# Optimization experiments

Hardware: AMD Instinct MI355X
Metric: run time of the kernel (lower is better)

## Reference

```python
import jax, jax.numpy as jnp
import numpy as np

H = 30  # hidden size
D_IN = 4
D_OUT = 4


def setup_inputs() -> dict:
    key = jax.random.key(0)
    ks = jax.random.split(key, 12)
    s = 0.1
    inp = {
        "input": jax.random.normal(ks[0], (2048, 1024, D_IN), dtype=jnp.float32),
        "W_ih1": jax.random.normal(ks[1], (4 * H, D_IN), dtype=jnp.float32) * s,
        "b_ih1": jax.random.normal(ks[2], (4 * H,), dtype=jnp.float32) * s,
        "W_hh1": jax.random.normal(ks[3], (4 * H, H), dtype=jnp.float32) * s,
        "b_hh1": jax.random.normal(ks[4], (4 * H,), dtype=jnp.float32) * s,
        "W_ih2": jax.random.normal(ks[5], (4 * H, H), dtype=jnp.float32) * s,
        "b_ih2": jax.random.normal(ks[6], (4 * H,), dtype=jnp.float32) * s,
        "W_hh2": jax.random.normal(ks[7], (4 * H, H), dtype=jnp.float32) * s,
        "b_hh2": jax.random.normal(ks[8], (4 * H,), dtype=jnp.float32) * s,
        "W_lin": jax.random.normal(ks[9], (D_OUT, H), dtype=jnp.float32) * s,
        "b_lin": jax.random.normal(ks[10], (D_OUT,), dtype=jnp.float32) * s,
        "future": 0,
    }
    return inp


def _lstm_cell(x, h, c, W_ih, b_ih, W_hh, b_hh):
    # PyTorch LSTMCell gate order: i, f, g, o
    gates = x @ W_ih.T + b_ih + h @ W_hh.T + b_hh  # [B, 4H]
    i, f, g, o = jnp.split(gates, 4, axis=-1)
    i = jax.nn.sigmoid(i)
    f = jax.nn.sigmoid(f)
    g = jnp.tanh(g)
    o = jax.nn.sigmoid(o)
    c_new = f * c + i * g
    h_new = o * jnp.tanh(c_new)
    return h_new, c_new


def reference(input, W_ih1, b_ih1, W_hh1, b_hh1, W_ih2, b_ih2, W_hh2, b_hh2,
              W_lin, b_lin, future):
    B, T, _ = input.shape

    def step(carry, x_t):
        h1, c1, h2, c2 = carry
        h1, c1 = _lstm_cell(x_t[:, :D_IN], h1, c1, W_ih1, b_ih1, W_hh1, b_hh1)
        h2, c2 = _lstm_cell(h1, h2, c2, W_ih2, b_ih2, W_hh2, b_hh2)
        out = h2 @ W_lin.T + b_lin  # [B, 4]
        return (h1, c1, h2, c2), out

    z = jnp.zeros((B, H), dtype=input.dtype)
    carry0 = (z, z, z, z)
    carry, outs = jax.lax.scan(step, carry0, jnp.transpose(input, (1, 0, 2)))
    outputs = jnp.transpose(outs, (1, 0, 2))  # [B, T, 4]

    if future > 0:
        h1, c1, h2, c2 = carry
        out = outputs[:, -1, :]
        fut = []
        for _ in range(future):
            h1, c1 = _lstm_cell(out, h1, c1, W_ih1, b_ih1, W_hh1, b_hh1)
            h2, c2 = _lstm_cell(h1, h2, c2, W_ih2, b_ih2, W_hh2, b_hh2)
            out = h2 @ W_lin.T + b_lin
            fut.append(out)
        outputs = jnp.concatenate([outputs, jnp.stack(fut, axis=1)], axis=1)
    return outputs
```

## Files before the change

kernel.cpp:

```cpp
#include <hip/hip_runtime.h>

typedef float f32x4 __attribute__((ext_vector_type(4)));
typedef float v4f  __attribute__((ext_vector_type(4)));
typedef _Float16 half8 __attribute__((ext_vector_type(8)));
typedef unsigned int u32;
typedef unsigned short u16;

#define HH 30
#define DIN 4
#define DOUT 4
#define NB 16
#define L2E 1.44269504088896340736f

#if __has_builtin(__builtin_amdgcn_exp2f)
#define EXP2F(v) __builtin_amdgcn_exp2f(v)
#else
#define EXP2F(v) exp2f(v)
#endif

__device__ __forceinline__ float sig2f(float v) {
    return __builtin_amdgcn_rcpf(1.0f + EXP2F(v));
}

__device__ __forceinline__ f32x4 MF(half8 a, half8 b, f32x4 c) {
    return __builtin_amdgcn_mfma_f32_16x16x32_f16(a, b, c, 0, 0, 0);
}

union F8 { half8 h; _Float16 e[8]; u32 w[4]; };
union HU { _Float16 h; u16 s; };

__device__ __forceinline__ void lds_barrier() {
    __builtin_amdgcn_sched_barrier(0);
    asm volatile("s_waitcnt lgkmcnt(0)" ::: "memory");
    __builtin_amdgcn_sched_barrier(0);
    __builtin_amdgcn_s_barrier();
    __builtin_amdgcn_sched_barrier(0);
}

__global__ __launch_bounds__(1024)
void lstm2_kernel(const float* __restrict__ x,
                  const float* __restrict__ Wih1, const float* __restrict__ bih1,
                  const float* __restrict__ Whh1, const float* __restrict__ bhh1,
                  const float* __restrict__ Wih2, const float* __restrict__ bih2,
                  const float* __restrict__ Whh2, const float* __restrict__ bhh2,
                  const float* __restrict__ Wlin, const float* __restrict__ blin,
                  float* __restrict__ out, int T)
{
    const int tid = threadIdx.x;
    const int w = tid >> 6;
    const int wt = w & 7;
    const bool isL2 = (w >= 8);
    const int l = tid & 63;
    const int n = l & 15;
    const int p = l >> 4;
    const int b0 = blockIdx.x * NB;
    const float M2 = -2.0f * L2E;

    __shared__ __align__(16) u16 lds[2][4][16][40];
    {
        u32* z = reinterpret_cast<u32*>(&lds[0][0][0][0]);
        const int tot = 2 * 4 * 16 * 40 / 2;
        for (int i = tid; i < tot; i += 1024) z[i] = 0u;
    }

    const int gA = n & 3;
    const float scA = (gA == 2) ? -2.0f * L2E : -L2E;
    const int qA = 4 * wt + (n >> 2);
    const int kq = 4 * wt + p;
    const bool okq = (kq < HH);
    const int kqc = okq ? kq : 0;
    const int pos = ((kq & 15) >> 2) * 8 + (kq >> 4) * 4 + (kq & 3);

    half8 wA_h0, wA_l0, wA_h1, wA_l1;
    {
        F8 H0, L0, H1, L1v;
#pragma unroll
        for (int e = 0; e < 8; ++e) {
            const int k = 16 * (e >> 2) + 4 * p + (e & 3);
            const bool kok = (qA < HH && k < HH);
            float v0, v1;
            if (isL2) {
                v0 = kok ? Wih2[(gA * HH + qA) * HH + k] * scA : 0.0f;
                v1 = kok ? Whh2[(gA * HH + qA) * HH + k] * scA : 0.0f;
            } else {
                v0 = kok ? Whh1[(gA * HH + qA) * HH + k] * scA : 0.0f;
                v1 = 0.0f;
            }
            _Float16 t0 = (_Float16)v0, t1 = (_Float16)v1;
            H0.e[e] = t0; L0.e[e] = (_Float16)(v0 - (float)t0);
            H1.e[e] = t1; L1v.e[e] = (_Float16)(v1 - (float)t1);
        }
        wA_h0 = H0.h; wA_l0 = L0.h; wA_h1 = H1.h; wA_l1 = L1v.h;
    }

    f32x4 biasf;
#pragma unroll
    for (int r = 0; r < 4; ++r) {
        const float scr = (r == 2) ? -2.0f * L2E : -L2E;
        const float bv = isL2 ? (bih2[r * HH + kqc] + bhh2[r * HH + kqc])
                              : (bih1[r * HH + kqc] + bhh1[r * HH + kqc]);
        biasf[r] = okq ? bv * scr : 0.0f;
    }

    float wxs[4][DIN];
#pragma unroll
    for (int r = 0; r < 4; ++r) {
        const float scr = (r == 2) ? -2.0f * L2E : -L2E;
#pragma unroll
        for (int c = 0; c < DIN; ++c)
            wxs[r][c] = (!isL2 && okq) ? Wih1[(r * HH + kqc) * DIN + c] * scr : 0.0f;
    }

    half8 alin_h, alin_l;
    f32x4 blinf;
    {
        F8 Lh, Ll;
#pragma unroll
        for (int e = 0; e < 8; ++e) {
            const int k = 16 * (e >> 2) + 4 * p + (e & 3);
            float v = (isL2 && n < DOUT && k < HH) ? Wlin[n * HH + k] : 0.0f;
            _Float16 t16 = (_Float16)v;
            Lh.e[e] = t16; Ll.e[e] = (_Float16)(v - (float)t16);
        }
        alin_h = Lh.h; alin_l = Ll.h;
#pragma unroll
        for (int r = 0; r < 4; ++r)
            blinf[r] = (p == 0) ? blin[r] : 0.0f;
    }

    float cst = 0.0f;
    half8 bh1_h = {}, bh1_l = {}, bh2_h = {}, bh2_l = {};

    const v4f* xp = reinterpret_cast<const v4f*>(x) + (size_t)(b0 + n) * T;

    f32x4 gx_cur = biasf;
    v4f xn = {};
    if (!isL2) {
        const v4f x0 = xp[0];
#pragma unroll
        for (int r = 0; r < 4; ++r)
#pragma unroll
            for (int c = 0; c < DIN; ++c)
                gx_cur[r] = fmaf(wxs[r][c], x0[c], gx_cur[r]);
        xn = xp[(T > 1) ? 1 : 0];
    }

    __syncthreads();

    const f32x4 zf = {0.0f, 0.0f, 0.0f, 0.0f};
    const int TS = T + 2;

    for (int s = 0; s < TS; ++s) {
        if (!isL2) {
            f32x4 a = MF(wA_h0, bh1_h, gx_cur);
            f32x4 b = MF(wA_h0, bh1_l, zf);
            f32x4 c = MF(wA_l0, bh1_h, zf);
            const f32x4 g = (a + b) + c;

            const float iv = sig2f(g[0]);
            const float fv = sig2f(g[1]);
            const float gg = fmaf(2.0f, sig2f(g[2]), -1.0f);
            const float ov = sig2f(g[3]);
            cst = fmaf(fv, cst, iv * gg);
            const float r = sig2f(M2 * cst);
            const float hn = fmaf(2.0f * ov, r, -ov);

            HU hi, lo;
            hi.h = (_Float16)hn;
            lo.h = (_Float16)(hn - (float)hi.h);
            lds[s & 1][0][n][pos] = okq ? hi.s : (u16)0;
            lds[s & 1][1][n][pos] = okq ? lo.s : (u16)0;
        } else {
            if (s >= 1) {
                f32x4 a = MF(wA_h0, bh1_h, biasf);
                f32x4 b = MF(wA_h0, bh1_l, zf);
                f32x4 c = MF(wA_l0, bh1_h, zf);
                f32x4 d = MF(wA_h1, bh2_h, zf);
                f32x4 e = MF(wA_h1, bh2_l, zf);
                f32x4 f = MF(wA_l1, bh2_h, zf);
                const f32x4 g = ((a + b) + (c + d)) + (e + f);

                const float iv = sig2f(g[0]);
                const float fv = sig2f(g[1]);
                const float gg = fmaf(2.0f, sig2f(g[2]), -1.0f);
                const float ov = sig2f(g[3]);
                cst = fmaf(fv, cst, iv * gg);
                const float r = sig2f(M2 * cst);
                const float hn = fmaf(2.0f * ov, r, -ov);

                HU hi, lo;
                hi.h = (_Float16)hn;
                lo.h = (_Float16)(hn - (float)hi.h);
                lds[(s + 1) & 1][2][n][pos] = okq ? hi.s : (u16)0;
                lds[(s + 1) & 1][3][n][pos] = okq ? lo.s : (u16)0;
            }
            if (s >= 2 && w == 8 + (s & 7)) {
                f32x4 oh = blinf;
                oh = MF(alin_h, bh2_h, oh);
                oh = MF(alin_h, bh2_l, oh);
                oh = MF(alin_l, bh2_h, oh);
                if (p == 0) {
                    v4f ov4;
                    ov4.x = oh[0]; ov4.y = oh[1]; ov4.z = oh[2]; ov4.w = oh[3];
                    *reinterpret_cast<v4f*>(
                        out + (((size_t)(b0 + n)) * T + (s - 2)) * DOUT) = ov4;
                }
            }
        }

        lds_barrier();

        bh1_h = *reinterpret_cast<const half8*>(&lds[s & 1][0][n][8 * p]);
        bh1_l = *reinterpret_cast<const half8*>(&lds[s & 1][1][n][8 * p]);
        if (isL2) {
            bh2_h = *reinterpret_cast<const half8*>(&lds[(s + 1) & 1][2][n][8 * p]);
            bh2_l = *reinterpret_cast<const half8*>(&lds[(s + 1) & 1][3][n][8 * p]);
        } else {
            f32x4 gxn = biasf;
#pragma unroll
            for (int r = 0; r < 4; ++r)
#pragma unroll
                for (int c = 0; c < DIN; ++c)
                    gxn[r] = fmaf(wxs[r][c], xn[c], gxn[r]);
            gx_cur = gxn;
            xn = xp[(s + 2 < T) ? (s + 2) : (T - 1)];
        }
    }
}

extern "C" void kernel_launch(void* const* d_in, const int* in_sizes, int n_in,
                              void* d_out, int out_size, void* d_ws, size_t ws_size,
                              hipStream_t stream)
{
    const float* x    = (const float*)d_in[0];
    const float* Wih1 = (const float*)d_in[1];
    const float* bih1 = (const float*)d_in[2];
    const float* Whh1 = (const float*)d_in[3];
    const float* bhh1 = (const float*)d_in[4];
    const float* Wih2 = (const float*)d_in[5];
    const float* bih2 = (const float*)d_in[6];
    const float* Whh2 = (const float*)d_in[7];
    const float* bhh2 = (const float*)d_in[8];
    const float* Wlin = (const float*)d_in[9];
    const float* blin = (const float*)d_in[10];
    float* out = (float*)d_out;

    const int T = 1024;
    const int B = in_sizes[0] / (T * DIN);

    hipLaunchKernelGGL(lstm2_kernel, dim3(B / NB), dim3(1024), 0, stream,
                       x, Wih1, bih1, Whh1, bhh1, Wih2, bih2, Whh2, bhh2,
                       Wlin, blin, out, T);
}
```

Baseline: 743.4 us.

## Halve block to 512 threads with each wave computing two row tiles

```diff
diff --git a/kernel.cpp b/kernel.cpp
--- a/kernel.cpp
+++ b/kernel.cpp
@@ -37,7 +37,7 @@
     __builtin_amdgcn_sched_barrier(0);
 }
 
-__global__ __launch_bounds__(1024)
+__global__ __launch_bounds__(512)
 void lstm2_kernel(const float* __restrict__ x,
                   const float* __restrict__ Wih1, const float* __restrict__ bih1,
                   const float* __restrict__ Whh1, const float* __restrict__ bhh1,
@@ -48,8 +48,8 @@
 {
     const int tid = threadIdx.x;
     const int w = tid >> 6;
-    const int wt = w & 7;
-    const bool isL2 = (w >= 8);
+    const int wg = w & 3;
+    const bool isL2 = (w >= 4);
     const int l = tid & 63;
     const int n = l & 15;
     const int p = l >> 4;
@@ -60,19 +60,27 @@
     {
         u32* z = reinterpret_cast<u32*>(&lds[0][0][0][0]);
         const int tot = 2 * 4 * 16 * 40 / 2;
-        for (int i = tid; i < tot; i += 1024) z[i] = 0u;
+        for (int i = tid; i < tot; i += 512) z[i] = 0u;
     }
 
     const int gA = n & 3;
     const float scA = (gA == 2) ? -2.0f * L2E : -L2E;
-    const int qA = 4 * wt + (n >> 2);
-    const int kq = 4 * wt + p;
-    const bool okq = (kq < HH);
-    const int kqc = okq ? kq : 0;
-    const int pos = ((kq & 15) >> 2) * 8 + (kq >> 4) * 4 + (kq & 3);
-
-    half8 wA_h0, wA_l0, wA_h1, wA_l1;
-    {
+
+    half8 wA_h0[2], wA_l0[2], wA_h1[2], wA_l1[2];
+    f32x4 biasf[2];
+    int pos_[2];
+    bool okq_[2];
+    int kqc_[2];
+
+#pragma unroll
+    for (int ri = 0; ri < 2; ++ri) {
+        const int rt = 2 * wg + ri;
+        const int qA = 4 * rt + (n >> 2);
+        const int kq = 4 * rt + p;
+        okq_[ri] = (kq < HH);
+        kqc_[ri] = okq_[ri] ? kq : 0;
+        pos_[ri] = ((kq & 15) >> 2) * 8 + (kq >> 4) * 4 + (kq & 3);
+
         F8 H0, L0, H1, L1v;
 #pragma unroll
         for (int e = 0; e < 8; ++e) {
@@ -90,26 +98,30 @@
             H0.e[e] = t0; L0.e[e] = (_Float16)(v0 - (float)t0);
             H1.e[e] = t1; L1v.e[e] = (_Float16)(v1 - (float)t1);
         }
-        wA_h0 = H0.h; wA_l0 = L0.h; wA_h1 = H1.h; wA_l1 = L1v.h;
-    }
-
-    f32x4 biasf;
-#pragma unroll
-    for (int r = 0; r < 4; ++r) {
-        const float scr = (r == 2) ? -2.0f * L2E : -L2E;
-        const float bv = isL2 ? (bih2[r * HH + kqc] + bhh2[r * HH + kqc])
-                              : (bih1[r * HH + kqc] + bhh1[r * HH + kqc]);
-        biasf[r] = okq ? bv * scr : 0.0f;
-    }
-
-    float wxs[4][DIN];
-#pragma unroll
-    for (int r = 0; r < 4; ++r) {
-        const float scr = (r == 2) ? -2.0f * L2E : -L2E;
-#pragma unroll
-        for (int c = 0; c < DIN; ++c)
-            wxs[r][c] = (!isL2 && okq) ? Wih1[(r * HH + kqc) * DIN + c] * scr : 0.0f;
-    }
+        wA_h0[ri] = H0.h; wA_l0[ri] = L0.h;
+        wA_h1[ri] = H1.h; wA_l1[ri] = L1v.h;
+
+#pragma unroll
+        for (int r = 0; r < 4; ++r) {
+            const float scr = (r == 2) ? -2.0f * L2E : -L2E;
+            const float bv = isL2
+                ? (bih2[r * HH + kqc_[ri]] + bhh2[r * HH + kqc_[ri]])
+                : (bih1[r * HH + kqc_[ri]] + bhh1[r * HH + kqc_[ri]]);
+            biasf[ri][r] = okq_[ri] ? bv * scr : 0.0f;
+        }
+    }
+
+    float wxs[2][4][DIN];
+#pragma unroll
+    for (int ri = 0; ri < 2; ++ri)
+#pragma unroll
+        for (int r = 0; r < 4; ++r) {
+            const float scr = (r == 2) ? -2.0f * L2E : -L2E;
+#pragma unroll
+            for (int c = 0; c < DIN; ++c)
+                wxs[ri][r][c] = (!isL2 && okq_[ri])
+                    ? Wih1[(r * HH + kqc_[ri]) * DIN + c] * scr : 0.0f;
+        }
 
     half8 alin_h, alin_l;
     f32x4 blinf;
@@ -128,20 +140,22 @@
             blinf[r] = (p == 0) ? blin[r] : 0.0f;
     }
 
-    float cst = 0.0f;
+    float cst0 = 0.0f, cst1 = 0.0f;
     half8 bh1_h = {}, bh1_l = {}, bh2_h = {}, bh2_l = {};
 
     const v4f* xp = reinterpret_cast<const v4f*>(x) + (size_t)(b0 + n) * T;
 
-    f32x4 gx_cur = biasf;
+    f32x4 gx0 = biasf[0], gx1 = biasf[1];
     v4f xn = {};
     if (!isL2) {
         const v4f x0 = xp[0];
 #pragma unroll
         for (int r = 0; r < 4; ++r)
 #pragma unroll
-            for (int c = 0; c < DIN; ++c)
-                gx_cur[r] = fmaf(wxs[r][c], x0[c], gx_cur[r]);
+            for (int c = 0; c < DIN; ++c) {
+                gx0[r] = fmaf(wxs[0][r][c], x0[c], gx0[r]);
+                gx1[r] = fmaf(wxs[1][r][c], x0[c], gx1[r]);
+            }
         xn = xp[(T > 1) ? 1 : 0];
     }
 
@@ -152,49 +166,58 @@
 
     for (int s = 0; s < TS; ++s) {
         if (!isL2) {
-            f32x4 a = MF(wA_h0, bh1_h, gx_cur);
-            f32x4 b = MF(wA_h0, bh1_l, zf);
-            f32x4 c = MF(wA_l0, bh1_h, zf);
-            const f32x4 g = (a + b) + c;
-
-            const float iv = sig2f(g[0]);
-            const float fv = sig2f(g[1]);
-            const float gg = fmaf(2.0f, sig2f(g[2]), -1.0f);
-            const float ov = sig2f(g[3]);
-            cst = fmaf(fv, cst, iv * gg);
-            const float r = sig2f(M2 * cst);
-            const float hn = fmaf(2.0f * ov, r, -ov);
-
-            HU hi, lo;
-            hi.h = (_Float16)hn;
-            lo.h = (_Float16)(hn - (float)hi.h);
-            lds[s & 1][0][n][pos] = okq ? hi.s : (u16)0;
-            lds[s & 1][1][n][pos] = okq ? lo.s : (u16)0;
-        } else {
-            if (s >= 1) {
-                f32x4 a = MF(wA_h0, bh1_h, biasf);
-                f32x4 b = MF(wA_h0, bh1_l, zf);
-                f32x4 c = MF(wA_l0, bh1_h, zf);
-                f32x4 d = MF(wA_h1, bh2_h, zf);
-                f32x4 e = MF(wA_h1, bh2_l, zf);
-                f32x4 f = MF(wA_l1, bh2_h, zf);
-                const f32x4 g = ((a + b) + (c + d)) + (e + f);
+#pragma unroll
+            for (int ri = 0; ri < 2; ++ri) {
+                const f32x4 gxc = ri ? gx1 : gx0;
+                f32x4 a = MF(wA_h0[ri], bh1_h, gxc);
+                f32x4 b = MF(wA_h0[ri], bh1_l, zf);
+                f32x4 c = MF(wA_l0[ri], bh1_h, zf);
+                const f32x4 g = (a + b) + c;
 
                 const float iv = sig2f(g[0]);
                 const float fv = sig2f(g[1]);
                 const float gg = fmaf(2.0f, sig2f(g[2]), -1.0f);
                 const float ov = sig2f(g[3]);
-                cst = fmaf(fv, cst, iv * gg);
-                const float r = sig2f(M2 * cst);
+                float& cs = ri ? cst1 : cst0;
+                cs = fmaf(fv, cs, iv * gg);
+                const float r = sig2f(M2 * cs);
                 const float hn = fmaf(2.0f * ov, r, -ov);
 
                 HU hi, lo;
                 hi.h = (_Float16)hn;
                 lo.h = (_Float16)(hn - (float)hi.h);
-                lds[(s + 1) & 1][2][n][pos] = okq ? hi.s : (u16)0;
-                lds[(s + 1) & 1][3][n][pos] = okq ? lo.s : (u16)0;
-            }
-            if (s >= 2 && w == 8 + (s & 7)) {
+                lds[s & 1][0][n][pos_[ri]] = okq_[ri] ? hi.s : (u16)0;
+                lds[s & 1][1][n][pos_[ri]] = okq_[ri] ? lo.s : (u16)0;
+            }
+        } else {
+            if (s >= 1) {
+#pragma unroll
+                for (int ri = 0; ri < 2; ++ri) {
+                    f32x4 a = MF(wA_h0[ri], bh1_h, biasf[ri]);
+                    f32x4 b = MF(wA_h0[ri], bh1_l, zf);
+                    f32x4 c = MF(wA_l0[ri], bh1_h, zf);
+                    f32x4 d = MF(wA_h1[ri], bh2_h, zf);
+                    f32x4 e = MF(wA_h1[ri], bh2_l, zf);
+                    f32x4 f = MF(wA_l1[ri], bh2_h, zf);
+                    const f32x4 g = ((a + b) + (c + d)) + (e + f);
+
+                    const float iv = sig2f(g[0]);
+                    const float fv = sig2f(g[1]);
+                    const float gg = fmaf(2.0f, sig2f(g[2]), -1.0f);
+                    const float ov = sig2f(g[3]);
+                    float& cs = ri ? cst1 : cst0;
+                    cs = fmaf(fv, cs, iv * gg);
+                    const float r = sig2f(M2 * cs);
+                    const float hn = fmaf(2.0f * ov, r, -ov);
+
+                    HU hi, lo;
+                    hi.h = (_Float16)hn;
+                    lo.h = (_Float16)(hn - (float)hi.h);
+                    lds[(s + 1) & 1][2][n][pos_[ri]] = okq_[ri] ? hi.s : (u16)0;
+                    lds[(s + 1) & 1][3][n][pos_[ri]] = okq_[ri] ? lo.s : (u16)0;
+                }
+            }
+            if (s >= 2 && w == 4 + (s & 3)) {
                 f32x4 oh = blinf;
                 oh = MF(alin_h, bh2_h, oh);
                 oh = MF(alin_h, bh2_l, oh);
@@ -216,13 +239,15 @@
             bh2_h = *reinterpret_cast<const half8*>(&lds[(s + 1) & 1][2][n][8 * p]);
             bh2_l = *reinterpret_cast<const half8*>(&lds[(s + 1) & 1][3][n][8 * p]);
         } else {
-            f32x4 gxn = biasf;
+            f32x4 g0 = biasf[0], g1 = biasf[1];
 #pragma unroll
             for (int r = 0; r < 4; ++r)
 #pragma unroll
-                for (int c = 0; c < DIN; ++c)
-                    gxn[r] = fmaf(wxs[r][c], xn[c], gxn[r]);
-            gx_cur = gxn;
+                for (int c = 0; c < DIN; ++c) {
+                    g0[r] = fmaf(wxs[0][r][c], xn[c], g0[r]);
+                    g1[r] = fmaf(wxs[1][r][c], xn[c], g1[r]);
+                }
+            gx0 = g0; gx1 = g1;
             xn = xp[(s + 2 < T) ? (s + 2) : (T - 1)];
         }
     }
@@ -248,7 +273,7 @@
     const int T = 1024;
     const int B = in_sizes[0] / (T * DIN);
 
-    hipLaunchKernelGGL(lstm2_kernel, dim3(B / NB), dim3(1024), 0, stream,
+    hipLaunchKernelGGL(lstm2_kernel, dim3(B / NB), dim3(512), 0, stream,
                        x, Wih1, bih1, Whh1, bhh1, Wih2, bih2, Whh2, bhh2,
                        Wlin, blin, out, T);
 }
```

After: 759.8 us. 1.02x slower.
